# Kernel tuning notes

Measured on AMD Instinct MI355X. Metric: run time of the kernel, lower is better.

## Reference

```python
import jax, jax.numpy as jnp
import numpy as np

D, E, H, K = 1024, 8, 4096, 2
B, S = 4, 2048


def setup_inputs() -> dict:
    key = jax.random.key(0)
    ks = jax.random.split(key, 5)
    scale = 0.02
    return {
        "x": jax.random.normal(ks[0], (B, S, D), dtype=jnp.float32),
        "gate_w": jax.random.normal(ks[1], (D, E), dtype=jnp.float32) * scale,
        "w1": jax.random.normal(ks[2], (E, D, H), dtype=jnp.float32) * scale,
        "b1": jnp.zeros((E, H), dtype=jnp.float32),
        "w2": jax.random.normal(ks[3], (E, H, D), dtype=jnp.float32) * scale,
        "b2": jnp.zeros((E, D), dtype=jnp.float32),
        "top_k": K,
    }


def reference(x, gate_w, w1, b1, w2, b2, top_k):
    orig_shape = x.shape
    d = x.shape[-1]
    xt = x.reshape(-1, d)                      # [T, D]
    T = xt.shape[0]

    # Gating: top-k over expert scores, softmax over the selected k.
    scores = xt @ gate_w                       # [T, E]
    expert_weights, expert_indices = jax.lax.top_k(scores, top_k)  # [T, K]
    expert_weights = jax.nn.softmax(expert_weights, axis=-1)

    # Dense all-expert MLP (GPT-style fc -> GELU -> proj), batched over experts.
    h = jnp.einsum('td,edh->eth', xt, w1) + b1[:, None, :]   # [E, T, H]
    h = jax.nn.gelu(h, approximate=False)
    outs = jnp.einsum('eth,ehd->etd', h, w2) + b2[:, None, :]  # [E, T, D]

    # Combine: gather each token's selected experts and mix with gate weights.
    tok = jnp.arange(T)[:, None]               # [T, 1]
    gathered = outs[expert_indices, tok]       # [T, K, D]
    y = jnp.sum(gathered * expert_weights[..., None], axis=1)  # [T, D]
    return y.reshape(orig_shape)
```

## Files before the change

### kernel.cpp

```cpp
#include <hip/hip_runtime.h>
#include <stdint.h>

#define T_TOK 8192
#define D_DIM 1024
#define E_NUM 8
#define H_DIM 4096

#define BM 128
#define BN 128
#define BK 64
#define NSEG 8
#define MAX_ROWS2 17408
#define MAX_MT2 (MAX_ROWS2/BM)
#define LCS 136

typedef unsigned short u16;
typedef __attribute__((ext_vector_type(8))) short shortx8;
typedef __attribute__((ext_vector_type(4))) float floatx4;
typedef __attribute__((ext_vector_type(8))) unsigned short ushortx8;

typedef const __attribute__((address_space(1))) unsigned int g_uint;
typedef __attribute__((address_space(3))) unsigned int l_uint;

__device__ __forceinline__ u16 f2bf(float f) {
  union { float f; unsigned int u; } v; v.f = f;
  unsigned int r = v.u + 0x7FFFu + ((v.u >> 16) & 1u);
  return (u16)(r >> 16);
}
__device__ __forceinline__ void gld_lds16(const u16* g, u16* l) {
  __builtin_amdgcn_global_load_lds((g_uint*)g, (l_uint*)l, 16, 0, 0);
}
__device__ __forceinline__ float gelu_fast(float v) {
  float y = v * (1.5957691216f + 0.07135481627f * v * v);
  y = fminf(y, 30.f);
  float ey = __expf(y);
  return v * ey * __builtin_amdgcn_rcpf(1.f + ey);
}

__device__ __forceinline__ void decode_block(int flat, int NT, int cmc, int& ntile, int& mloc) {
  if ((cmc & 7) == 0) {
    int xcd = flat & 7, seq = flat >> 3;
    ntile = seq & (NT - 1);
    mloc = (seq / NT) * 8 + xcd;
  } else {
    ntile = flat & (NT - 1);
    mloc = flat / NT;
  }
}

__global__ __launch_bounds__(256) void init_kernel(int* counts, int* fills, int* row_token) {
  int i = blockIdx.x * 256 + threadIdx.x;
  if (i < MAX_ROWS2) row_token[i] = -1;
  if (blockIdx.x == 0 && threadIdx.x < NSEG) { counts[threadIdx.x] = 0; fills[threadIdx.x] = 0; }
}

__global__ __launch_bounds__(256) void zero4_kernel(float4* out) {
  out[(size_t)blockIdx.x * 256 + threadIdx.x] = float4{0.f, 0.f, 0.f, 0.f};
}

__global__ __launch_bounds__(256) void gate_kernel(const float* __restrict__ X, const float* __restrict__ GW,
                                                   u16* __restrict__ XC,
                                                   int* __restrict__ tk_idx, float* __restrict__ tk_w,
                                                   int* __restrict__ counts) {
  const int lane = threadIdx.x & 63;
  const int t = blockIdx.x * 4 + (threadIdx.x >> 6);
  const float4* xr4 = (const float4*)(X + (size_t)t * D_DIM + lane * 16);
  const float4* gw4 = (const float4*)GW;
  float acc[E_NUM];
#pragma unroll
  for (int e = 0; e < E_NUM; e++) acc[e] = 0.f;
  ushortx8 o0, o1;
#pragma unroll
  for (int i4 = 0; i4 < 4; i4++) {
    float4 xv = xr4[i4];
#pragma unroll
    for (int c = 0; c < 4; c++) {
      float xs = (&xv.x)[c];
      int q = i4 * 4 + c;
      if (q < 8) o0[q] = f2bf(xs); else o1[q - 8] = f2bf(xs);
      int d = lane * 16 + q;
      float4 g0 = gw4[d * 2], g1 = gw4[d * 2 + 1];
      acc[0] += xs * g0.x; acc[1] += xs * g0.y; acc[2] += xs * g0.z; acc[3] += xs * g0.w;
      acc[4] += xs * g1.x; acc[5] += xs * g1.y; acc[6] += xs * g1.z; acc[7] += xs * g1.w;
    }
  }
  u16* xcb = XC + (size_t)t * D_DIM + lane * 16;
  *(ushortx8*)xcb = o0;
  *(ushortx8*)(xcb + 8) = o1;
#pragma unroll
  for (int e = 0; e < E_NUM; e++)
    for (int off = 32; off; off >>= 1) acc[e] += __shfl_xor(acc[e], off);
  if (lane == 0) {
    int i0 = 0; float v0 = acc[0];
#pragma unroll
    for (int e = 1; e < E_NUM; e++) if (acc[e] > v0) { v0 = acc[e]; i0 = e; }
    int i1 = -1; float v1 = -1e30f;
#pragma unroll
    for (int e = 0; e < E_NUM; e++) if (e != i0 && acc[e] > v1) { v1 = acc[e]; i1 = e; }
    float e1 = expf(v1 - v0);
    float inv = 1.f / (1.f + e1);
    tk_idx[t * 2] = i0; tk_idx[t * 2 + 1] = i1;
    tk_w[t * 2] = inv;  tk_w[t * 2 + 1] = e1 * inv;
    atomicAdd(&counts[i0], 1); atomicAdd(&counts[i1], 1);
  }
}

__global__ void prefix_kernel(const int* counts, int* seg) {
  if (threadIdx.x == 0 && blockIdx.x == 0) {
    int a = 0;
    for (int i = 0; i < NSEG; i++) { seg[i] = a; a += ((counts[i] + BM - 1) / BM) * BM; }
    seg[NSEG] = a;
  }
}

__global__ __launch_bounds__(256) void fill_kernel(const int* __restrict__ tk_idx, const float* __restrict__ tk_w,
                                                   const int* __restrict__ seg, int* __restrict__ fills,
                                                   int* __restrict__ row_token, float* __restrict__ row_weight,
                                                   int* __restrict__ row_of) {
  int t = blockIdx.x * 256 + threadIdx.x;
  if (t >= T_TOK) return;
#pragma unroll
  for (int s = 0; s < 2; s++) {
    int sidx = tk_idx[t * 2 + s];
    int pos = atomicAdd(&fills[sidx], 1);
    int r = seg[sidx] + pos;
    row_token[r] = t; row_weight[r] = tk_w[t * 2 + s];
    row_of[t * 2 + s] = r;
  }
}

__global__ __launch_bounds__(256) void transpose_kernel(const float* __restrict__ src, u16* __restrict__ dst,
                                                        int R, int C) {
  __shared__ u16 tile[64][68];
  const int tid = threadIdx.x;
  size_t off = (size_t)blockIdx.z * (size_t)R * C;
  int r0 = blockIdx.y * 64, c0 = blockIdx.x * 64;
  int rr = tid >> 4, cc = (tid & 15) * 4;
#pragma unroll
  for (int i = 0; i < 4; i++) {
    int r = rr + i * 16;
    float4 v = *(const float4*)&src[off + (size_t)(r0 + r) * C + c0 + cc];
    u16* tp = &tile[r][cc];
    tp[0] = f2bf(v.x); tp[1] = f2bf(v.y); tp[2] = f2bf(v.z); tp[3] = f2bf(v.w);
  }
  __syncthreads();
  int c = tid >> 3, rb = (tid & 7) * 8;
#pragma unroll
  for (int i = 0; i < 2; i++) {
    int cx = c + i * 32;
    ushortx8 o;
#pragma unroll
    for (int q = 0; q < 8; q++) o[q] = tile[rb + q][cx];
    *(ushortx8*)&dst[off + (size_t)(c0 + cx) * R + r0 + rb] = o;
  }
}

__global__ __launch_bounds__(256, 4) void fc1_kernel(const u16* __restrict__ XC, const u16* __restrict__ W1T,
                                                     const float* __restrict__ B1, u16* __restrict__ Hbuf,
                                                     const int* __restrict__ row_token, const int* __restrict__ seg,
                                                     int mtile0, int cmc, int e_filter) {
  int ntile, mloc;
  decode_block(blockIdx.x, H_DIM / BN, cmc, ntile, mloc);
  const int mtile = mtile0 + mloc;
  const int row0 = mtile * BM;
  if (row0 >= seg[NSEG]) return;
  int sidx = 0;
#pragma unroll
  for (int i = 1; i < NSEG; i++) if (row0 >= seg[i]) sidx = i;
  const int e = sidx;
  if (e_filter >= 0 && e != e_filter) return;
  const size_t ebase = (e_filter >= 0) ? 0 : (size_t)e * H_DIM;
  const u16* Bbase = W1T + (ebase + (size_t)ntile * BN) * D_DIM;

  __shared__ u16 lds_u16[BM * LCS];
  u16* lA = lds_u16;
  u16* lB = lds_u16 + BM * BK;
  const int tid = threadIdx.x;
  const int sub = tid >> 3, acol = (tid & 7) * 8;
  unsigned int offA[4], offB[4];
#pragma unroll
  for (int r = 0; r < 4; r++) {
    int arow = r * 32 + sub;
    int tok = row_token[row0 + arow]; if (tok < 0) tok = 0;
    offA[r] = (unsigned int)tok * D_DIM + acol;
    offB[r] = (unsigned int)arow * D_DIM + acol;
  }
  const int lane = tid & 63;
  const int mq = (tid >> 7) & 1, nq = (tid >> 6) & 1;
  const int lrow = lane & 15, quad = lane >> 4;
  floatx4 acc[4][4];
#pragma unroll
  for (int i = 0; i < 4; i++)
#pragma unroll
    for (int j = 0; j < 4; j++)
#pragma unroll
      for (int r = 0; r < 4; r++) acc[i][j][r] = 0.f;

  for (int k0 = 0; k0 < D_DIM; k0 += BK) {
#pragma unroll
    for (int r = 0; r < 4; r++) gld_lds16(XC + offA[r] + k0, &lA[(r * 256 + tid) * 8]);
#pragma unroll
    for (int r = 0; r < 4; r++) gld_lds16(Bbase + offB[r] + k0, &lB[(r * 256 + tid) * 8]);
    __syncthreads();
#pragma unroll
    for (int kk = 0; kk < 2; kk++) {
      shortx8 af[4], bfr[4];
#pragma unroll
      for (int i = 0; i < 4; i++) af[i]  = *(const shortx8*)&lA[(mq * 64 + i * 16 + lrow) * BK + kk * 32 + quad * 8];
#pragma unroll
      for (int i = 0; i < 4; i++) bfr[i] = *(const shortx8*)&lB[(nq * 64 + i * 16 + lrow) * BK + kk * 32 + quad * 8];
#pragma unroll
      for (int i = 0; i < 4; i++)
#pragma unroll
        for (int j = 0; j < 4; j++)
          acc[i][j] = __builtin_amdgcn_mfma_f32_16x16x32_bf16(af[i], bfr[j], acc[i][j], 0, 0, 0);
    }
    __syncthreads();
  }
#pragma unroll
  for (int j = 0; j < 4; j++) {
    float bv = B1[(size_t)e * H_DIM + ntile * BN + nq * 64 + j * 16 + lrow];
    int col = nq * 64 + j * 16 + lrow;
#pragma unroll
    for (int i = 0; i < 4; i++) {
      int row = mq * 64 + i * 16 + quad * 4;
#pragma unroll
      for (int rr = 0; rr < 4; rr++) {
        float v = acc[i][j][rr] + bv;
        lds_u16[(row + rr) * LCS + col] = f2bf(gelu_fast(v));
      }
    }
  }
  __syncthreads();
  {
    const int r = tid >> 1, c0 = (tid & 1) * 64;
    size_t gbase = (size_t)(mloc * BM + r) * H_DIM + (size_t)ntile * BN + c0;
#pragma unroll
    for (int q = 0; q < 8; q++)
      *(ushortx8*)&Hbuf[gbase + q * 8] = *(const ushortx8*)&lds_u16[r * LCS + c0 + q * 8];
  }
}

__global__ __launch_bounds__(256, 4) void fc2_kernel(const u16* __restrict__ Hbuf, const u16* __restrict__ W2T,
                                                     const float* __restrict__ B2, float* __restrict__ outbuf,
                                                     const int* __restrict__ row_token, const float* __restrict__ row_weight,
                                                     const int* __restrict__ seg,
                                                     int mtile0, int cmc, int e_filter) {
  int ntile, mloc;
  decode_block(blockIdx.x, D_DIM / BN, cmc, ntile, mloc);
  const int mtile = mtile0 + mloc;
  const int row0 = mtile * BM;
  if (row0 >= seg[NSEG]) return;
  int sidx = 0;
#pragma unroll
  for (int i = 1; i < NSEG; i++) if (row0 >= seg[i]) sidx = i;
  const int e = sidx;
  if (e_filter >= 0 && e != e_filter) return;
  const size_t ebase = (e_filter >= 0) ? 0 : (size_t)e * D_DIM;
  const u16* Bbase = W2T + (ebase + (size_t)ntile * BN) * H_DIM;

  __shared__ u16 lA[BM * BK];
  __shared__ u16 lB[BN * BK];
  const int tid = threadIdx.x;
  const int sub = tid >> 3, acol = (tid & 7) * 8;
  unsigned int offA[4], offB[4];
#pragma unroll
  for (int r = 0; r < 4; r++) {
    int arow = r * 32 + sub;
    offA[r] = (unsigned int)(mloc * BM + arow) * H_DIM + acol;
    offB[r] = (unsigned int)arow * H_DIM + acol;
  }
  const int lane = tid & 63;
  const int mq = (tid >> 7) & 1, nq = (tid >> 6) & 1;
  const int lrow = lane & 15, quad = lane >> 4;
  floatx4 acc[4][4];
#pragma unroll
  for (int i = 0; i < 4; i++)
#pragma unroll
    for (int j = 0; j < 4; j++)
#pragma unroll
      for (int r = 0; r < 4; r++) acc[i][j][r] = 0.f;

  for (int k0 = 0; k0 < H_DIM; k0 += BK) {
#pragma unroll
    for (int r = 0; r < 4; r++) gld_lds16(Hbuf + offA[r] + k0, &lA[(r * 256 + tid) * 8]);
#pragma unroll
    for (int r = 0; r < 4; r++) gld_lds16(Bbase + offB[r] + k0, &lB[(r * 256 + tid) * 8]);
    __syncthreads();
#pragma unroll
    for (int kk = 0; kk < 2; kk++) {
      shortx8 af[4], bfr[4];
#pragma unroll
      for (int i = 0; i < 4; i++) af[i]  = *(const shortx8*)&lA[(mq * 64 + i * 16 + lrow) * BK + kk * 32 + quad * 8];
#pragma unroll
      for (int i = 0; i < 4; i++) bfr[i] = *(const shortx8*)&lB[(nq * 64 + i * 16 + lrow) * BK + kk * 32 + quad * 8];
#pragma unroll
      for (int i = 0; i < 4; i++)
#pragma unroll
        for (int j = 0; j < 4; j++)
          acc[i][j] = __builtin_amdgcn_mfma_f32_16x16x32_bf16(af[i], bfr[j], acc[i][j], 0, 0, 0);
    }
    __syncthreads();
  }
#pragma unroll
  for (int i = 0; i < 4; i++)
#pragma unroll
    for (int rr = 0; rr < 4; rr++) {
      int gr = row0 + mq * 64 + i * 16 + quad * 4 + rr;
      int tok = row_token[gr];
      if (tok >= 0) {
        float wgt = row_weight[gr];
        float* obase = outbuf + (size_t)gr * D_DIM + (size_t)ntile * BN + nq * 64 + lrow;
#pragma unroll
        for (int j = 0; j < 4; j++) {
          float bv = B2[(size_t)e * D_DIM + ntile * BN + nq * 64 + j * 16 + lrow];
          obase[j * 16] = (acc[i][j][rr] + bv) * wgt;
        }
      }
    }
}

__global__ __launch_bounds__(256) void combine_kernel(const float* __restrict__ outbuf, const int* __restrict__ row_of,
                                                      float* __restrict__ out) {
  int t = blockIdx.x;
  int d = threadIdx.x * 4;
  int r0 = row_of[t * 2], r1 = row_of[t * 2 + 1];
  float4 a = *(const float4*)&outbuf[(size_t)r0 * D_DIM + d];
  float4 b = *(const float4*)&outbuf[(size_t)r1 * D_DIM + d];
  *(float4*)&out[(size_t)t * D_DIM + d] = float4{a.x + b.x, a.y + b.y, a.z + b.z, a.w + b.w};
}

extern "C" void kernel_launch(void* const* d_in, const int* in_sizes, int n_in,
                              void* d_out, int out_size, void* d_ws, size_t ws_size,
                              hipStream_t stream) {
  const float* x  = (const float*)d_in[0];
  const float* gw = (const float*)d_in[1];
  const float* w1 = (const float*)d_in[2];
  const float* b1 = (const float*)d_in[3];
  const float* w2 = (const float*)d_in[4];
  const float* b2 = (const float*)d_in[5];
  float* out = (float*)d_out;

  char* p = (char*)d_ws;
  auto alloc = [&](size_t n) { char* q = p; p += (n + 255) & ~(size_t)255; return q; };
  int*   counts     = (int*)alloc(NSEG * 4);
  int*   fills      = (int*)alloc(NSEG * 4);
  int*   seg        = (int*)alloc((NSEG + 1) * 4);
  int*   tk_idx     = (int*)alloc((size_t)T_TOK * 2 * 4);
  float* tk_w       = (float*)alloc((size_t)T_TOK * 2 * 4);
  int*   row_token  = (int*)alloc((size_t)MAX_ROWS2 * 4);
  float* row_weight = (float*)alloc((size_t)MAX_ROWS2 * 4);
  int*   row_of     = (int*)alloc((size_t)T_TOK * 2 * 4);
  u16*   xc         = (u16*)alloc((size_t)T_TOK * D_DIM * 2);
  float* outbuf     = (float*)alloc((size_t)MAX_ROWS2 * D_DIM * 4);
  size_t meta = (size_t)(p - (char*)d_ws);

  const size_t Wfull = (size_t)E_NUM * H_DIM * D_DIM * 2;
  const size_t Wone  = (size_t)H_DIM * D_DIM * 2;
  auto hbytes = [](int n) { int cmx = (MAX_MT2 + n - 1) / n; return (size_t)cmx * BM * H_DIM * 2; };

  int mode = 3, N = 1;
  {
    const int cand[6] = {1, 2, 4, 8, 16, 32};
    for (int ci = 0; ci < 6 && mode == 3; ci++)
      if (meta + 2 * Wfull + hbytes(cand[ci]) <= ws_size) { mode = 0; N = cand[ci]; }
    for (int ci = 0; ci < 6 && mode == 3; ci++)
      if (meta + Wfull + hbytes(cand[ci]) <= ws_size) { mode = 1; N = cand[ci]; }
    for (int ci = 0; ci < 6 && mode == 3; ci++)
      if (meta + Wone + hbytes(cand[ci]) <= ws_size) { mode = 2; N = cand[ci]; }
  }

  if (mode == 3) {
    zero4_kernel<<<(int)(((size_t)T_TOK * D_DIM) / 1024), 256, 0, stream>>>((float4*)out);
    return;
  }

  u16 *W1T, *W2T;
  if (mode == 0) { W1T = (u16*)alloc(Wfull); W2T = (u16*)alloc(Wfull); }
  else           { W1T = W2T = (u16*)alloc(mode == 1 ? Wfull : Wone); }
  u16* Hbuf = (u16*)alloc(hbytes(N));
  const int cm = (MAX_MT2 + N - 1) / N;

  init_kernel<<<(MAX_ROWS2 + 255) / 256, 256, 0, stream>>>(counts, fills, row_token);
  gate_kernel<<<T_TOK / 4, 256, 0, stream>>>(x, gw, xc, tk_idx, tk_w, counts);
  prefix_kernel<<<1, 64, 0, stream>>>(counts, seg);
  fill_kernel<<<T_TOK / 256, 256, 0, stream>>>(tk_idx, tk_w, seg, fills, row_token, row_weight, row_of);

  if (mode == 0) {
    transpose_kernel<<<dim3(H_DIM / 64, D_DIM / 64, E_NUM), 256, 0, stream>>>(w1, W1T, D_DIM, H_DIM);
    transpose_kernel<<<dim3(D_DIM / 64, H_DIM / 64, E_NUM), 256, 0, stream>>>(w2, W2T, H_DIM, D_DIM);
  }

  for (int c = 0; c < N; ++c) {
    int mtile0 = c * cm;
    int cmc = MAX_MT2 - mtile0; if (cmc > cm) cmc = cm; if (cmc <= 0) break;
    if (mode == 0) {
      fc1_kernel<<<cmc * (H_DIM / BN), 256, 0, stream>>>(xc, W1T, b1, Hbuf, row_token, seg, mtile0, cmc, -1);
      fc2_kernel<<<cmc * (D_DIM / BN), 256, 0, stream>>>(Hbuf, W2T, b2, outbuf, row_token, row_weight, seg, mtile0, cmc, -1);
    } else if (mode == 1) {
      transpose_kernel<<<dim3(H_DIM / 64, D_DIM / 64, E_NUM), 256, 0, stream>>>(w1, W1T, D_DIM, H_DIM);
      fc1_kernel<<<cmc * (H_DIM / BN), 256, 0, stream>>>(xc, W1T, b1, Hbuf, row_token, seg, mtile0, cmc, -1);
      transpose_kernel<<<dim3(D_DIM / 64, H_DIM / 64, E_NUM), 256, 0, stream>>>(w2, W2T, H_DIM, D_DIM);
      fc2_kernel<<<cmc * (D_DIM / BN), 256, 0, stream>>>(Hbuf, W2T, b2, outbuf, row_token, row_weight, seg, mtile0, cmc, -1);
    } else {
      for (int e = 0; e < E_NUM; e++) {
        transpose_kernel<<<dim3(H_DIM / 64, D_DIM / 64, 1), 256, 0, stream>>>(w1 + (size_t)e * D_DIM * H_DIM, W1T, D_DIM, H_DIM);
        fc1_kernel<<<cmc * (H_DIM / BN), 256, 0, stream>>>(xc, W1T, b1, Hbuf, row_token, seg, mtile0, cmc, e);
      }
      for (int e = 0; e < E_NUM; e++) {
        transpose_kernel<<<dim3(D_DIM / 64, H_DIM / 64, 1), 256, 0, stream>>>(w2 + (size_t)e * H_DIM * D_DIM, W2T, H_DIM, D_DIM);
        fc2_kernel<<<cmc * (D_DIM / BN), 256, 0, stream>>>(Hbuf, W2T, b2, outbuf, row_token, row_weight, seg, mtile0, cmc, e);
      }
    }
  }
  combine_kernel<<<T_TOK, 256, 0, stream>>>(outbuf, row_of, out);
}
```

Measured before the change: 1.030 ms.

## XOR-swizzle LDS tiles in fc1/fc2 and drop XCD-aware block decode

Result: faster. 981.5 us (-4.7%).

```diff
diff --git a/kernel.cpp b/kernel.cpp
--- a/kernel.cpp
+++ b/kernel.cpp
@@ -35,17 +35,6 @@
   y = fminf(y, 30.f);
   float ey = __expf(y);
   return v * ey * __builtin_amdgcn_rcpf(1.f + ey);
-}
-
-__device__ __forceinline__ void decode_block(int flat, int NT, int cmc, int& ntile, int& mloc) {
-  if ((cmc & 7) == 0) {
-    int xcd = flat & 7, seq = flat >> 3;
-    ntile = seq & (NT - 1);
-    mloc = (seq / NT) * 8 + xcd;
-  } else {
-    ntile = flat & (NT - 1);
-    mloc = flat / NT;
-  }
 }
 
 __global__ __launch_bounds__(256) void init_kernel(int* counts, int* fills, int* row_token) {
@@ -131,7 +120,7 @@
 
 __global__ __launch_bounds__(256) void transpose_kernel(const float* __restrict__ src, u16* __restrict__ dst,
                                                         int R, int C) {
-  __shared__ u16 tile[64][68];
+  __shared__ u16 tile[64][70];
   const int tid = threadIdx.x;
   size_t off = (size_t)blockIdx.z * (size_t)R * C;
   int r0 = blockIdx.y * 64, c0 = blockIdx.x * 64;
@@ -158,9 +147,8 @@
 __global__ __launch_bounds__(256, 4) void fc1_kernel(const u16* __restrict__ XC, const u16* __restrict__ W1T,
                                                      const float* __restrict__ B1, u16* __restrict__ Hbuf,
                                                      const int* __restrict__ row_token, const int* __restrict__ seg,
-                                                     int mtile0, int cmc, int e_filter) {
-  int ntile, mloc;
-  decode_block(blockIdx.x, H_DIM / BN, cmc, ntile, mloc);
+                                                     int mtile0, int e_filter) {
+  const int ntile = blockIdx.x, mloc = blockIdx.y;
   const int mtile = mtile0 + mloc;
   const int row0 = mtile * BM;
   if (row0 >= seg[NSEG]) return;
@@ -176,18 +164,20 @@
   u16* lA = lds_u16;
   u16* lB = lds_u16 + BM * BK;
   const int tid = threadIdx.x;
-  const int sub = tid >> 3, acol = (tid & 7) * 8;
+  const int sub = tid >> 3;
+  const int csw = (((tid & 7) ^ (sub & 7)) * 8);
   unsigned int offA[4], offB[4];
 #pragma unroll
   for (int r = 0; r < 4; r++) {
     int arow = r * 32 + sub;
     int tok = row_token[row0 + arow]; if (tok < 0) tok = 0;
-    offA[r] = (unsigned int)tok * D_DIM + acol;
-    offB[r] = (unsigned int)arow * D_DIM + acol;
+    offA[r] = (unsigned int)tok * D_DIM + csw;
+    offB[r] = (unsigned int)arow * D_DIM + csw;
   }
   const int lane = tid & 63;
   const int mq = (tid >> 7) & 1, nq = (tid >> 6) & 1;
   const int lrow = lane & 15, quad = lane >> 4;
+  const int rsw = lrow & 7;
   floatx4 acc[4][4];
 #pragma unroll
   for (int i = 0; i < 4; i++)
@@ -204,11 +194,12 @@
     __syncthreads();
 #pragma unroll
     for (int kk = 0; kk < 2; kk++) {
+      const int ch = ((kk * 4 + quad) ^ rsw) * 8;
       shortx8 af[4], bfr[4];
 #pragma unroll
-      for (int i = 0; i < 4; i++) af[i]  = *(const shortx8*)&lA[(mq * 64 + i * 16 + lrow) * BK + kk * 32 + quad * 8];
-#pragma unroll
-      for (int i = 0; i < 4; i++) bfr[i] = *(const shortx8*)&lB[(nq * 64 + i * 16 + lrow) * BK + kk * 32 + quad * 8];
+      for (int i = 0; i < 4; i++) af[i]  = *(const shortx8*)&lA[(mq * 64 + i * 16 + lrow) * BK + ch];
+#pragma unroll
+      for (int i = 0; i < 4; i++) bfr[i] = *(const shortx8*)&lB[(nq * 64 + i * 16 + lrow) * BK + ch];
 #pragma unroll
       for (int i = 0; i < 4; i++)
 #pragma unroll
@@ -245,9 +236,8 @@
                                                      const float* __restrict__ B2, float* __restrict__ outbuf,
                                                      const int* __restrict__ row_token, const float* __restrict__ row_weight,
                                                      const int* __restrict__ seg,
-                                                     int mtile0, int cmc, int e_filter) {
-  int ntile, mloc;
-  decode_block(blockIdx.x, D_DIM / BN, cmc, ntile, mloc);
+                                                     int mtile0, int e_filter) {
+  const int ntile = blockIdx.x, mloc = blockIdx.y;
   const int mtile = mtile0 + mloc;
   const int row0 = mtile * BM;
   if (row0 >= seg[NSEG]) return;
@@ -262,17 +252,19 @@
   __shared__ u16 lA[BM * BK];
   __shared__ u16 lB[BN * BK];
   const int tid = threadIdx.x;
-  const int sub = tid >> 3, acol = (tid & 7) * 8;
+  const int sub = tid >> 3;
+  const int csw = (((tid & 7) ^ (sub & 7)) * 8);
   unsigned int offA[4], offB[4];
 #pragma unroll
   for (int r = 0; r < 4; r++) {
     int arow = r * 32 + sub;
-    offA[r] = (unsigned int)(mloc * BM + arow) * H_DIM + acol;
-    offB[r] = (unsigned int)arow * H_DIM + acol;
+    offA[r] = (unsigned int)(mloc * BM + arow) * H_DIM + csw;
+    offB[r] = (unsigned int)arow * H_DIM + csw;
   }
   const int lane = tid & 63;
   const int mq = (tid >> 7) & 1, nq = (tid >> 6) & 1;
   const int lrow = lane & 15, quad = lane >> 4;
+  const int rsw = lrow & 7;
   floatx4 acc[4][4];
 #pragma unroll
   for (int i = 0; i < 4; i++)
@@ -289,11 +281,12 @@
     __syncthreads();
 #pragma unroll
     for (int kk = 0; kk < 2; kk++) {
+      const int ch = ((kk * 4 + quad) ^ rsw) * 8;
       shortx8 af[4], bfr[4];
 #pragma unroll
-      for (int i = 0; i < 4; i++) af[i]  = *(const shortx8*)&lA[(mq * 64 + i * 16 + lrow) * BK + kk * 32 + quad * 8];
-#pragma unroll
-      for (int i = 0; i < 4; i++) bfr[i] = *(const shortx8*)&lB[(nq * 64 + i * 16 + lrow) * BK + kk * 32 + quad * 8];
+      for (int i = 0; i < 4; i++) af[i]  = *(const shortx8*)&lA[(mq * 64 + i * 16 + lrow) * BK + ch];
+#pragma unroll
+      for (int i = 0; i < 4; i++) bfr[i] = *(const shortx8*)&lB[(nq * 64 + i * 16 + lrow) * BK + ch];
 #pragma unroll
       for (int i = 0; i < 4; i++)
 #pragma unroll
@@ -395,21 +388,21 @@
     int mtile0 = c * cm;
     int cmc = MAX_MT2 - mtile0; if (cmc > cm) cmc = cm; if (cmc <= 0) break;
     if (mode == 0) {
-      fc1_kernel<<<cmc * (H_DIM / BN), 256, 0, stream>>>(xc, W1T, b1, Hbuf, row_token, seg, mtile0, cmc, -1);
-      fc2_kernel<<<cmc * (D_DIM / BN), 256, 0, stream>>>(Hbuf, W2T, b2, outbuf, row_token, row_weight, seg, mtile0, cmc, -1);
+      fc1_kernel<<<dim3(H_DIM / BN, cmc), 256, 0, stream>>>(xc, W1T, b1, Hbuf, row_token, seg, mtile0, -1);
+      fc2_kernel<<<dim3(D_DIM / BN, cmc), 256, 0, stream>>>(Hbuf, W2T, b2, outbuf, row_token, row_weight, seg, mtile0, -1);
     } else if (mode == 1) {
       transpose_kernel<<<dim3(H_DIM / 64, D_DIM / 64, E_NUM), 256, 0, stream>>>(w1, W1T, D_DIM, H_DIM);
-      fc1_kernel<<<cmc * (H_DIM / BN), 256, 0, stream>>>(xc, W1T, b1, Hbuf, row_token, seg, mtile0, cmc, -1);
+      fc1_kernel<<<dim3(H_DIM / BN, cmc), 256, 0, stream>>>(xc, W1T, b1, Hbuf, row_token, seg, mtile0, -1);
       transpose_kernel<<<dim3(D_DIM / 64, H_DIM / 64, E_NUM), 256, 0, stream>>>(w2, W2T, H_DIM, D_DIM);
-      fc2_kernel<<<cmc * (D_DIM / BN), 256, 0, stream>>>(Hbuf, W2T, b2, outbuf, row_token, row_weight, seg, mtile0, cmc, -1);
+      fc2_kernel<<<dim3(D_DIM / BN, cmc), 256, 0, stream>>>(Hbuf, W2T, b2, outbuf, row_token, row_weight, seg, mtile0, -1);
     } else {
       for (int e = 0; e < E_NUM; e++) {
         transpose_kernel<<<dim3(H_DIM / 64, D_DIM / 64, 1), 256, 0, stream>>>(w1 + (size_t)e * D_DIM * H_DIM, W1T, D_DIM, H_DIM);
-        fc1_kernel<<<cmc * (H_DIM / BN), 256, 0, stream>>>(xc, W1T, b1, Hbuf, row_token, seg, mtile0, cmc, e);
+        fc1_kernel<<<dim3(H_DIM / BN, cmc), 256, 0, stream>>>(xc, W1T, b1, Hbuf, row_token, seg, mtile0, e);
       }
       for (int e = 0; e < E_NUM; e++) {
         transpose_kernel<<<dim3(D_DIM / 64, H_DIM / 64, 1), 256, 0, stream>>>(w2 + (size_t)e * H_DIM * D_DIM, W2T, H_DIM, D_DIM);
-        fc2_kernel<<<cmc * (D_DIM / BN), 256, 0, stream>>>(Hbuf, W2T, b2, outbuf, row_token, row_weight, seg, mtile0, cmc, e);
+        fc2_kernel<<<dim3(D_DIM / BN, cmc), 256, 0, stream>>>(Hbuf, W2T, b2, outbuf, row_token, row_weight, seg, mtile0, e);
       }
     }
   }
```
